# Performance work log

Measured on AMD Instinct MI355X. Metric: run time of the kernel, lower is better.

The kernel has to match this reference:

```python
import jax, jax.numpy as jnp
import numpy as np

D_MODEL = 1024
NUM_HEADS = 16
HEAD_DIM = D_MODEL // NUM_HEADS  # 64
ROPE_THETA = 10000.0
SEQ_LEN = 4096
BATCH = 1


def apply_rope(x, positions, theta=ROPE_THETA):
    # x: [b, h, s, d], positions: [s]
    d = x.shape[-1]
    inv_freq = theta ** (-jnp.arange(0, d, 2, dtype=jnp.float32) / d)  # [d/2]
    angles = positions.astype(jnp.float32)[:, None] * inv_freq[None, :]  # [s, d/2]
    cos = jnp.cos(angles)  # [s, d/2]
    sin = jnp.sin(angles)
    x1 = x[..., 0::2]  # [b, h, s, d/2]
    x2 = x[..., 1::2]
    r1 = x1 * cos - x2 * sin
    r2 = x1 * sin + x2 * cos
    # interleave back to [..., d]
    out = jnp.stack([r1, r2], axis=-1).reshape(x.shape)
    return out.astype(x.dtype)


def setup_inputs() -> dict:
    key = jax.random.key(0)
    k_x, k_qkv, k_o = jax.random.split(key, 3)
    scale_in = 1.0 / np.sqrt(D_MODEL)
    return {
        "x": jax.random.normal(k_x, (BATCH, SEQ_LEN, D_MODEL), dtype=jnp.float32),
        "token_positions": jnp.arange(SEQ_LEN, dtype=jnp.int64 if jax.config.jax_enable_x64 else jnp.int32),
        "w_qkv": jax.random.normal(k_qkv, (3 * D_MODEL, D_MODEL), dtype=jnp.float32) * scale_in,
        "w_o": jax.random.normal(k_o, (D_MODEL, D_MODEL), dtype=jnp.float32) * scale_in,
    }


def reference(x, token_positions, w_qkv, w_o):
    b, s, _ = x.shape
    # QKV projection (Linear without bias, weight [out, in])
    x_qkv = jnp.einsum('bsd,ed->bse', x, w_qkv)  # [b, s, 3*d_model]
    # rearrange 'b s (three heads kv) -> three b heads s kv'
    x_qkv = x_qkv.reshape(b, s, 3, NUM_HEADS, HEAD_DIM)
    x_qkv = jnp.transpose(x_qkv, (2, 0, 3, 1, 4))  # [3, b, h, s, d]
    q, k, v = x_qkv[0], x_qkv[1], x_qkv[2]
    q = apply_rope(q, token_positions)
    k = apply_rope(k, token_positions)
    # scaled dot-product attention with causal mask
    scores = jnp.einsum('bhnd,bhmd->bhnm', q, k) / jnp.sqrt(jnp.float32(HEAD_DIM))
    causal = jnp.tril(jnp.ones((s, s), dtype=bool))  # [s, s]
    scores = jnp.where(causal[None, None], scores, jnp.float32(-jnp.inf))
    weights = jax.nn.softmax(scores, axis=-1)
    attn = jnp.einsum('bhnm,bhmd->bhnd', weights, v)  # [b, h, s, d]
    attn = jnp.transpose(attn, (0, 2, 1, 3)).reshape(b, s, NUM_HEADS * HEAD_DIM)
    return jnp.einsum('bsd,ed->bse', attn, w_o)
```

## Files before the change

kernel.cpp:

```cpp
#include <hip/hip_runtime.h>

#define SEQ 4096
#define DMODEL 1024
#define HEADS 16
#define HD 64
#define NQKV 3072

typedef __attribute__((ext_vector_type(8))) __bf16 bf16x8;
typedef __attribute__((ext_vector_type(4))) __bf16 bf16x4;
typedef __attribute__((ext_vector_type(8))) short short8;
typedef __attribute__((ext_vector_type(4))) float f32x4;
typedef __attribute__((ext_vector_type(16))) float f32x16;
typedef __attribute__((ext_vector_type(4))) unsigned int u32x4;

__device__ __forceinline__ unsigned short f2bf(float f) {
    unsigned u = __builtin_bit_cast(unsigned, f);
    return (unsigned short)((u + 0x7fffu + ((u >> 16) & 1u)) >> 16);
}
__device__ __forceinline__ float bf2f(unsigned short h) {
    return __builtin_bit_cast(float, (unsigned)h << 16);
}
__device__ __forceinline__ unsigned cvt_pk_bf16(float lo, float hi) {
    unsigned r;
    asm("v_cvt_pk_bf16_f32 %0, %1, %2" : "=v"(r) : "v"(lo), "v"(hi));
    return r;
}

__device__ __forceinline__ void gload16(const void* g, void* l) {
    __builtin_amdgcn_global_load_lds(
        (const __attribute__((address_space(1))) unsigned int*)g,
        (__attribute__((address_space(3))) unsigned int*)l, 16, 0, 0);
}

#define TS(qt, kh) (0x40 | ((kh) << 5) | (qt))
__device__ __constant__ unsigned char TASKS[28] = {
    TS(15,0), TS(15,1), TS(14,0), TS(14,1), TS(13,0), TS(13,1),
    TS(12,0), TS(12,1), TS(11,0), TS(11,1), TS(10,0), TS(10,1),
    TS(9,0),  TS(9,1),  TS(8,0),  TS(8,1),  TS(7,0),  TS(7,1),
    3,        TS(6,0),  TS(6,1),  2,        TS(5,0),  TS(5,1),
    TS(4,0),  TS(4,1),  1,        0
};

__global__ void f2bf_all(const float* __restrict__ x, const float* __restrict__ wqkv,
                         const float* __restrict__ wo, unsigned short* __restrict__ dst) {
    const int N0 = SEQ * DMODEL / 4;
    const int N1 = N0 + NQKV * DMODEL / 4;
    const int NT = N1 + DMODEL * DMODEL / 4;
    int i = blockIdx.x * 256 + threadIdx.x;
    int stride = gridDim.x * 256;
    for (; i < NT; i += stride) {
        const float4* src;
        if (i < N0)      src = reinterpret_cast<const float4*>(x) + i;
        else if (i < N1) src = reinterpret_cast<const float4*>(wqkv) + (i - N0);
        else             src = reinterpret_cast<const float4*>(wo) + (i - N1);
        float4 f = *src;
        ushort4 o;
        o.x = f2bf(f.x); o.y = f2bf(f.y); o.z = f2bf(f.z); o.w = f2bf(f.w);
        reinterpret_cast<ushort4*>(dst)[i] = o;
    }
}

template <int EPI>
__global__ __launch_bounds__(256) void gemm_bt(const unsigned short* __restrict__ A,
                                               const unsigned short* __restrict__ B,
                                               float* __restrict__ outF,
                                               unsigned short* __restrict__ outB,
                                               int M, int N, int K) {
    alignas(16) __shared__ unsigned short a_lds[2][128 * 32];
    alignas(16) __shared__ unsigned short b_lds[2][128 * 32];
    const int tid = threadIdx.x;
    const int wave = tid >> 6, lane = tid & 63;
    const int l16 = lane & 15, g = lane >> 4;
    const int wr = wave >> 1, wc = wave & 1;
    const int bm = blockIdx.x, bn = blockIdx.y;

    const int lrow = lane >> 2;
    const int lcol = (lane & 3) * 8;

    const unsigned short* Ag = A + (size_t)(bm * 128 + lrow) * K + lcol;
    const unsigned short* Bg = B + (size_t)(bn * 128 + lrow) * K + lcol;

    f32x4 acc[4][4] = {};
    const int NS = K / 32;

    auto STAGE = [&](int b, int ks) {
#pragma unroll
        for (int j = 0; j < 2; ++j) {
            int chunk = wave * 2 + j;
            gload16(Ag + (size_t)(chunk * 16) * K + ks * 32, a_lds[b] + chunk * 512);
            gload16(Bg + (size_t)(chunk * 16) * K + ks * 32, b_lds[b] + chunk * 512);
        }
    };

    STAGE(0, 0);

    for (int ks = 0; ks < NS; ++ks) {
        const int cur = ks & 1;
        asm volatile("s_waitcnt vmcnt(0)" ::: "memory");
        __builtin_amdgcn_s_barrier();
        if (ks + 1 < NS) STAGE(cur ^ 1, ks + 1);

        bf16x8 af[4], bfr[4];
#pragma unroll
        for (int m = 0; m < 4; ++m)
            af[m] = *reinterpret_cast<const bf16x8*>(a_lds[cur] + (wr * 64 + m * 16 + l16) * 32 + g * 8);
#pragma unroll
        for (int n = 0; n < 4; ++n)
            bfr[n] = *reinterpret_cast<const bf16x8*>(b_lds[cur] + (wc * 64 + n * 16 + l16) * 32 + g * 8);
        __builtin_amdgcn_s_setprio(1);
#pragma unroll
        for (int m = 0; m < 4; ++m)
#pragma unroll
            for (int n = 0; n < 4; ++n)
                acc[m][n] = __builtin_amdgcn_mfma_f32_16x16x32_bf16(af[m], bfr[n], acc[m][n], 0, 0, 0);
        __builtin_amdgcn_s_setprio(0);
    }

#pragma unroll
    for (int m = 0; m < 4; ++m)
#pragma unroll
        for (int n = 0; n < 4; ++n)
#pragma unroll
            for (int r = 0; r < 4; ++r) {
                int row = bm * 128 + wr * 64 + m * 16 + g * 4 + r;
                int col = bn * 128 + wc * 64 + n * 16 + l16;
                float v = acc[m][n][r];
                if (EPI == 0) {
                    int part = col >> 10;
                    int hd = col & 1023;
                    int h = hd >> 6, d = hd & 63;
                    outB[(size_t)((part * HEADS + h) * SEQ + row) * HD + d] = f2bf(v);
                } else {
                    outF[(size_t)row * N + col] = v;
                }
            }
}

__global__ __launch_bounds__(256) void rope_kernel(unsigned short* qkv, const int* __restrict__ pos) {
    int idx = blockIdx.x * 256 + threadIdx.x;
    int chunk = idx & 7;
    int row = idx >> 3;
    int s = row & (SEQ - 1);
    int ph = row >> 12;
    float p = (float)pos[s];
    float scale = (ph < HEADS) ? 0.125f * 1.4426950408889634f : 1.0f;
    unsigned short* base = qkv + ((size_t)ph * SEQ + s) * HD + chunk * 8;
    short8 v = *reinterpret_cast<short8*>(base);
    short8 o;
    const float k = -13.287712379549449f / 32.0f;
#pragma unroll
    for (int j = 0; j < 4; ++j) {
        int i = chunk * 4 + j;
        float ang = p * exp2f((float)i * k);
        float sn, cs;
        sincosf(ang, &sn, &cs);
        float x1 = bf2f((unsigned short)v[2 * j]);
        float x2 = bf2f((unsigned short)v[2 * j + 1]);
        o[2 * j]     = (short)f2bf((x1 * cs - x2 * sn) * scale);
        o[2 * j + 1] = (short)f2bf((x1 * sn + x2 * cs) * scale);
    }
    *reinterpret_cast<short8*>(base) = o;
}

__global__ __launch_bounds__(256) void transpose_v(const unsigned short* __restrict__ qkv,
                                                   unsigned short* __restrict__ vt) {
    const int st = blockIdx.x;
    const int h = blockIdx.y;
    __shared__ unsigned short tile[64][72];
    const unsigned short* Vg = qkv + (size_t)((2 * HEADS + h) * SEQ) * HD;
    const int tid = threadIdx.x;
#pragma unroll
    for (int j = 0; j < 2; ++j) {
        int b = (tid + j * 256) * 8;
        int row = b >> 6;
        int col = b & 63;
        short8 v = *reinterpret_cast<const short8*>(Vg + (size_t)(st * 64 + row) * HD + col);
#pragma unroll
        for (int i = 0; i < 8; ++i) tile[row][col + i] = (unsigned short)v[i];
    }
    __syncthreads();
#pragma unroll
    for (int j = 0; j < 2; ++j) {
        int b = (tid + j * 256) * 8;
        int d = b >> 6;
        int sc = b & 63;
        short8 o;
#pragma unroll
        for (int i = 0; i < 8; ++i) o[i] = (short)tile[sc + i][d];
        *reinterpret_cast<short8*>(vt + (size_t)(h * HD + d) * SEQ + st * 64 + sc) = o;
    }
}

__global__ __launch_bounds__(512) void attn_kernel(const unsigned short* __restrict__ qkv,
                                                   const unsigned short* __restrict__ vt,
                                                   unsigned short* __restrict__ attnout,
                                                   int* __restrict__ qcnt,
                                                   unsigned short* __restrict__ pO,
                                                   float* __restrict__ lmf) {
    const int xcd = blockIdx.x & 7;
    const int tid = threadIdx.x;
    const int wave = tid >> 6, lane = tid & 63;
    const int l32 = lane & 31, hi = lane >> 5;

    alignas(16) __shared__ unsigned short k_lds[2][128 * 64];
    alignas(16) __shared__ unsigned short v_lds[2][2][64 * 64];
    __shared__ int slot_sh;

    const int rsw = (l32 & 7) << 4;

    for (;;) {
        if (tid == 0) slot_sh = atomicAdd(&qcnt[xcd], 1);
        __syncthreads();
        const int t = slot_sh;
        __syncthreads();
        if (t >= 56) break;

        const int hloc = t & 1;
        const unsigned char e = TASKS[t >> 1];
        const int qtile = e & 31;
        const int khalf = (e >> 5) & 1;
        const bool isSplit = (e >> 6) != 0;
        const int T = 2 * qtile + 2, Hh = qtile + 1;
        const int k0 = isSplit ? (khalf ? Hh : 0) : 0;
        const int k1 = isSplit ? (khalf ? T : Hh) : T;
        const int h = xcd * 2 + hloc;

        const unsigned short* Qg = qkv + (size_t)((0 * HEADS + h) * SEQ) * HD;
        const unsigned short* Kg = qkv + (size_t)((1 * HEADS + h) * SEQ) * HD;
        const unsigned short* VTg = vt + (size_t)h * HD * SEQ;

        const int qbase = qtile * 256 + wave * 32;
        const int qrow = qbase + l32;

        bf16x8 qf[4];
#pragma unroll
        for (int dg = 0; dg < 4; ++dg)
            qf[dg] = *reinterpret_cast<const bf16x8*>(Qg + (size_t)qrow * HD + dg * 16 + hi * 8);

        f32x16 oa[2] = {};
        float m_r = -1e30f, l_r = 0.f;

        auto STAGE = [&](int b, int kt) {
#pragma unroll
            for (int i = 0; i < 2; ++i) {
                int base = wave * 2048 + i * 1024;
                int byte = base + lane * 16;
                int krow = byte >> 7;
                int kc8 = ((byte >> 4) & 7) ^ (krow & 7);
                gload16(Kg + (size_t)(kt * 128 + krow) * HD + kc8 * 8, (char*)k_lds[b] + base);
                int fr = byte >> 7;
                int h64 = fr >> 6, vd = fr & 63;
                int vc8 = ((byte >> 4) & 7) ^ (vd & 7);
                gload16(VTg + (size_t)vd * SEQ + kt * 128 + h64 * 64 + vc8 * 8,
                        (char*)v_lds[b] + base);
            }
        };

        STAGE(0, k0);

        for (int kt = k0; kt < k1; ++kt) {
            const int cur = (kt - k0) & 1;
            asm volatile("s_waitcnt vmcnt(0)" ::: "memory");
            __builtin_amdgcn_s_barrier();
            if (kt + 1 < k1) STAGE(cur ^ 1, kt + 1);

#pragma unroll
            for (int hh = 0; hh < 2; ++hh) {
                if (hh && (kt * 128 + 64) > (qbase + 31)) break;

                f32x16 s[2] = {};
                __builtin_amdgcn_s_setprio(1);
#pragma unroll
                for (int g = 0; g < 2; ++g) {
                    int row = hh * 64 + g * 32 + l32;
#pragma unroll
                    for (int dg = 0; dg < 4; ++dg) {
                        bf16x8 kf = *reinterpret_cast<const bf16x8*>(
                            (char*)k_lds[cur] + row * 128 + ((dg * 32 + hi * 16) ^ rsw));
                        s[g] = __builtin_amdgcn_mfma_f32_32x32x16_bf16(kf, qf[dg], s[g], 0, 0, 0);
                    }
                }
                __builtin_amdgcn_s_setprio(0);

                if (kt * 128 + hh * 64 + 63 > qbase) {
#pragma unroll
                    for (int g = 0; g < 2; ++g)
#pragma unroll
                        for (int r = 0; r < 16; ++r) {
                            int kv = kt * 128 + hh * 64 + g * 32 + (r & 3) + 8 * (r >> 2) + 4 * hi;
                            if (kv > qrow) s[g][r] = -1e30f;
                        }
                }

                float ma = -1e30f, mb = -1e30f, mc = -1e30f, md = -1e30f;
#pragma unroll
                for (int r = 0; r < 16; r += 4) {
                    ma = fmaxf(ma, fmaxf(s[0][r], s[1][r]));
                    mb = fmaxf(mb, fmaxf(s[0][r + 1], s[1][r + 1]));
                    mc = fmaxf(mc, fmaxf(s[0][r + 2], s[1][r + 2]));
                    md = fmaxf(md, fmaxf(s[0][r + 3], s[1][r + 3]));
                }
                float mx = fmaxf(fmaxf(ma, mb), fmaxf(mc, md));
                mx = fmaxf(mx, __shfl_xor(mx, 32));

                if (__any(mx > m_r + 8.0f)) {
                    float mnew = fmaxf(m_r, mx);
                    float alpha = __builtin_amdgcn_exp2f(m_r - mnew);
                    m_r = mnew;
#pragma unroll
                    for (int r = 0; r < 16; ++r) { oa[0][r] *= alpha; oa[1][r] *= alpha; }
                    l_r *= alpha;
                }

#pragma unroll
                for (int g = 0; g < 2; ++g)
#pragma unroll
                    for (int r = 0; r < 16; ++r) s[g][r] = __builtin_amdgcn_exp2f(s[g][r] - m_r);

                float ra = 0.f, rb = 0.f;
#pragma unroll
                for (int r = 0; r < 16; r += 2) {
                    ra += s[0][r] + s[1][r];
                    rb += s[0][r + 1] + s[1][r + 1];
                }
                float rs = ra + rb;
                rs += __shfl_xor(rs, 32);
                l_r += rs;

                __builtin_amdgcn_s_setprio(1);
#pragma unroll
                for (int g = 0; g < 2; ++g) {
                    u32x4 pfw[2];
#pragma unroll
                    for (int u = 0; u < 2; ++u) {
                        unsigned wA = cvt_pk_bf16(s[g][8 * u + 0], s[g][8 * u + 1]);
                        unsigned wC = cvt_pk_bf16(s[g][8 * u + 2], s[g][8 * u + 3]);
                        unsigned wB = cvt_pk_bf16(s[g][8 * u + 4], s[g][8 * u + 5]);
                        unsigned wD = cvt_pk_bf16(s[g][8 * u + 6], s[g][8 * u + 7]);
                        unsigned wAx = __shfl_xor((int)wA, 32), wBx = __shfl_xor((int)wB, 32);
                        unsigned wCx = __shfl_xor((int)wC, 32), wDx = __shfl_xor((int)wD, 32);
                        pfw[u][0] = hi ? wBx : wA;
                        pfw[u][1] = hi ? wDx : wC;
                        pfw[u][2] = hi ? wB : wAx;
                        pfw[u][3] = hi ? wD : wCx;
                    }
#pragma unroll
                    for (int u = 0; u < 2; ++u) {
                        bf16x8 pf = __builtin_bit_cast(bf16x8, pfw[u]);
                        int ks = g * 2 + u;
#pragma unroll
                        for (int dg = 0; dg < 2; ++dg) {
                            bf16x8 vf = *reinterpret_cast<const bf16x8*>(
                                (char*)v_lds[cur][hh] + (dg * 32 + l32) * 128 + ((ks * 32 + hi * 16) ^ rsw));
                            oa[dg] = __builtin_amdgcn_mfma_f32_32x32x16_bf16(vf, pf, oa[dg], 0, 0, 0);
                        }
                    }
                }
                __builtin_amdgcn_s_setprio(0);
            }
        }

        const int ql = wave * 32 + l32;
        if (isSplit) {
            int sidx = (h * 12 + (qtile - 4)) * 2 + khalf;
            unsigned short* Op = pO + (size_t)sidx * 16384;
#pragma unroll
            for (int dg = 0; dg < 2; ++dg)
#pragma unroll
                for (int rq = 0; rq < 4; ++rq) {
                    ushort4 ov;
                    ov.x = f2bf(oa[dg][4 * rq + 0]);
                    ov.y = f2bf(oa[dg][4 * rq + 1]);
                    ov.z = f2bf(oa[dg][4 * rq + 2]);
                    ov.w = f2bf(oa[dg][4 * rq + 3]);
                    *reinterpret_cast<ushort4*>(Op + ql * 64 + dg * 32 + 8 * rq + 4 * hi) = ov;
                }
            if (hi == 0) {
                lmf[sidx * 512 + ql] = l_r;
                lmf[sidx * 512 + 256 + ql] = m_r;
            }
        } else {
            float inv = 1.0f / l_r;
            unsigned short* orow = attnout + (size_t)(qtile * 256 + ql) * DMODEL + h * HD;
#pragma unroll
            for (int dg = 0; dg < 2; ++dg)
#pragma unroll
                for (int rq = 0; rq < 4; ++rq) {
                    ushort4 ov;
                    ov.x = f2bf(oa[dg][4 * rq + 0] * inv);
                    ov.y = f2bf(oa[dg][4 * rq + 1] * inv);
                    ov.z = f2bf(oa[dg][4 * rq + 2] * inv);
                    ov.w = f2bf(oa[dg][4 * rq + 3] * inv);
                    *reinterpret_cast<ushort4*>(orow + dg * 32 + 8 * rq + 4 * hi) = ov;
                }
        }
    }
}

__global__ __launch_bounds__(256) void merge_kernel(const unsigned short* __restrict__ pO,
                                                    const float* __restrict__ lmf,
                                                    unsigned short* __restrict__ attnout) {
    int idx = blockIdx.x * 256 + threadIdx.x;
    if (idx >= 16 * 12 * 2048) return;
    int h = idx / (12 * 2048);
    int r = idx % (12 * 2048);
    int qt = r >> 11;
    int rr = r & 2047;
    int q = rr >> 3, d8 = rr & 7;

    int s0 = (h * 12 + qt) * 2;
    float l0 = lmf[s0 * 512 + q],       m0 = lmf[s0 * 512 + 256 + q];
    float l1 = lmf[(s0 + 1) * 512 + q], m1 = lmf[(s0 + 1) * 512 + 256 + q];
    float m = fmaxf(m0, m1);
    float a0 = __builtin_amdgcn_exp2f(m0 - m), a1 = __builtin_amdgcn_exp2f(m1 - m);
    float L = l0 * a0 + l1 * a1;
    float c0 = a0 / L, c1 = a1 / L;

    const unsigned short* O0 = pO + (size_t)s0 * 16384 + q * 64 + d8 * 8;
    const unsigned short* O1 = O0 + 16384;
    short8 v0 = *reinterpret_cast<const short8*>(O0);
    short8 v1 = *reinterpret_cast<const short8*>(O1);
    short8 o;
#pragma unroll
    for (int j = 0; j < 8; ++j) {
        float val = bf2f((unsigned short)v0[j]) * c0 + bf2f((unsigned short)v1[j]) * c1;
        o[j] = (short)f2bf(val);
    }
    int qtile = qt + 4;
    *reinterpret_cast<short8*>(attnout + (size_t)(qtile * 256 + q) * DMODEL + h * HD + d8 * 8) = o;
}

extern "C" void kernel_launch(void* const* d_in, const int* in_sizes, int n_in,
                              void* d_out, int out_size, void* d_ws, size_t ws_size,
                              hipStream_t stream) {
    const float* x = (const float*)d_in[0];
    const int* pos = (const int*)d_in[1];
    const float* wqkv = (const float*)d_in[2];
    const float* wo = (const float*)d_in[3];
    float* out = (float*)d_out;

    unsigned short* xb = (unsigned short*)d_ws;
    unsigned short* wqkvb = xb + (size_t)SEQ * DMODEL;
    unsigned short* wob = wqkvb + (size_t)NQKV * DMODEL;
    unsigned short* qkvp = wob + (size_t)DMODEL * DMODEL;
    unsigned short* vt = qkvp + (size_t)3 * HEADS * SEQ * HD;
    unsigned short* attnb = vt + (size_t)HEADS * HD * SEQ;

    char* sbase = (char*)d_ws;
    int* qcnt = (int*)sbase;
    float* lmf = (float*)(sbase + 1024);
    unsigned short* pO = (unsigned short*)(sbase + (1 << 20));

    f2bf_all<<<2048, 256, 0, stream>>>(x, wqkv, wo, xb);

    dim3 g1(SEQ / 128, NQKV / 128);
    gemm_bt<0><<<g1, 256, 0, stream>>>(xb, wqkvb, nullptr, qkvp, SEQ, NQKV, DMODEL);

    rope_kernel<<<(2 * HEADS * SEQ * 8) / 256, 256, 0, stream>>>(qkvp, pos);
    transpose_v<<<dim3(SEQ / 64, HEADS), 256, 0, stream>>>(qkvp, vt);

    hipMemsetAsync(qcnt, 0, 64, stream);
    attn_kernel<<<512, 512, 0, stream>>>(qkvp, vt, attnb, qcnt, pO, lmf);
    merge_kernel<<<(16 * 12 * 2048 + 255) / 256, 256, 0, stream>>>(pO, lmf, attnb);

    dim3 g2(SEQ / 128, DMODEL / 128);
    gemm_bt<1><<<g2, 256, 0, stream>>>(attnb, wob, out, nullptr, SEQ, DMODEL, DMODEL);
}
```

Before: 147.2 us.

## Fuse RoPE and V transpose into QKV GEMM epilogue with precomputed sin/cos

Removes the separate rope and transpose_v kernels by applying RoPE (with the Q scale) directly to fp32 accumulators in the QKV GEMM epilogue, pairing adjacent columns with a lane shuffle. V tiles are transposed through a small LDS buffer and written straight into the transposed layout. Sin/cos tables are precomputed in the conversion kernel. This saves two launches and a full read/write of the Q, K and V buffers, and RoPE now rounds once from fp32 instead of twice. In exchange the epilogue does more per-element table loads and scattered 2-byte stores, and the V path has no barrier around the per-wave LDS tile.

```diff
diff --git a/kernel.cpp b/kernel.cpp
--- a/kernel.cpp
+++ b/kernel.cpp
@@ -42,7 +42,9 @@
 };
 
 __global__ void f2bf_all(const float* __restrict__ x, const float* __restrict__ wqkv,
-                         const float* __restrict__ wo, unsigned short* __restrict__ dst) {
+                         const float* __restrict__ wo, const int* __restrict__ pos,
+                         unsigned short* __restrict__ dst,
+                         float* __restrict__ csT, float* __restrict__ snT) {
     const int N0 = SEQ * DMODEL / 4;
     const int N1 = N0 + NQKV * DMODEL / 4;
     const int NT = N1 + DMODEL * DMODEL / 4;
@@ -58,6 +60,16 @@
         o.x = f2bf(f.x); o.y = f2bf(f.y); o.z = f2bf(f.z); o.w = f2bf(f.w);
         reinterpret_cast<ushort4*>(dst)[i] = o;
     }
+    const float kk = -13.287712379549449f / 32.0f;
+    for (int idx = blockIdx.x * 256 + threadIdx.x; idx < SEQ * 32; idx += stride) {
+        int s = idx >> 5, fi = idx & 31;
+        float p = (float)pos[s];
+        float ang = p * exp2f((float)fi * kk);
+        float sn_, cs_;
+        sincosf(ang, &sn_, &cs_);
+        csT[idx] = cs_;
+        snT[idx] = sn_;
+    }
 }
 
 template <int EPI>
@@ -65,9 +77,13 @@
                                                const unsigned short* __restrict__ B,
                                                float* __restrict__ outF,
                                                unsigned short* __restrict__ outB,
+                                               unsigned short* __restrict__ vtp,
+                                               const float* __restrict__ csT,
+                                               const float* __restrict__ snT,
                                                int M, int N, int K) {
     alignas(16) __shared__ unsigned short a_lds[2][128 * 32];
     alignas(16) __shared__ unsigned short b_lds[2][128 * 32];
+    __shared__ unsigned short vtile[4][16][72];
     const int tid = threadIdx.x;
     const int wave = tid >> 6, lane = tid & 63;
     const int l16 = lane & 15, g = lane >> 4;
@@ -116,78 +132,55 @@
         __builtin_amdgcn_s_setprio(0);
     }
 
-#pragma unroll
-    for (int m = 0; m < 4; ++m)
-#pragma unroll
-        for (int n = 0; n < 4; ++n)
-#pragma unroll
-            for (int r = 0; r < 4; ++r) {
-                int row = bm * 128 + wr * 64 + m * 16 + g * 4 + r;
-                int col = bn * 128 + wc * 64 + n * 16 + l16;
-                float v = acc[m][n][r];
-                if (EPI == 0) {
-                    int part = col >> 10;
-                    int hd = col & 1023;
-                    int h = hd >> 6, d = hd & 63;
-                    outB[(size_t)((part * HEADS + h) * SEQ + row) * HD + d] = f2bf(v);
-                } else {
-                    outF[(size_t)row * N + col] = v;
+    if (EPI == 0) {
+        const float QS = 0.125f * 1.4426950408889634f;
+#pragma unroll
+        for (int n = 0; n < 4; ++n) {
+            const int col = bn * 128 + wc * 64 + n * 16 + l16;
+            const int part = col >> 10;
+            const int hh = (col >> 6) & 15;
+            const int d = n * 16 + l16;
+            if (part < 2) {
+                const int fi = (col & 63) >> 1;
+                const float sc = (part == 0) ? QS : 1.0f;
+                const bool odd = (col & 1) != 0;
+#pragma unroll
+                for (int m = 0; m < 4; ++m)
+#pragma unroll
+                    for (int r = 0; r < 4; ++r) {
+                        int row = bm * 128 + wr * 64 + m * 16 + g * 4 + r;
+                        float v = acc[m][n][r];
+                        float pp = __shfl_xor(v, 1);
+                        float cs_ = csT[row * 32 + fi];
+                        float sn_ = snT[row * 32 + fi];
+                        float out = odd ? (pp * sn_ + v * cs_) : (v * cs_ - pp * sn_);
+                        outB[(size_t)((part * HEADS + hh) * SEQ + row) * HD + (col & 63)] = f2bf(out * sc);
+                    }
+            } else {
+#pragma unroll
+                for (int m = 0; m < 4; ++m)
+#pragma unroll
+                    for (int r = 0; r < 4; ++r)
+                        vtile[wave][l16][m * 16 + g * 4 + r] = f2bf(acc[m][n][r]);
+#pragma unroll
+                for (int dd = 0; dd < 16; ++dd) {
+                    int dg = ((col & 63) & ~15) + dd;
+                    vtp[(size_t)(hh * HD + dg) * SEQ + bm * 128 + wr * 64 + lane] =
+                        vtile[wave][dd][lane];
                 }
             }
-}
-
-__global__ __launch_bounds__(256) void rope_kernel(unsigned short* qkv, const int* __restrict__ pos) {
-    int idx = blockIdx.x * 256 + threadIdx.x;
-    int chunk = idx & 7;
-    int row = idx >> 3;
-    int s = row & (SEQ - 1);
-    int ph = row >> 12;
-    float p = (float)pos[s];
-    float scale = (ph < HEADS) ? 0.125f * 1.4426950408889634f : 1.0f;
-    unsigned short* base = qkv + ((size_t)ph * SEQ + s) * HD + chunk * 8;
-    short8 v = *reinterpret_cast<short8*>(base);
-    short8 o;
-    const float k = -13.287712379549449f / 32.0f;
-#pragma unroll
-    for (int j = 0; j < 4; ++j) {
-        int i = chunk * 4 + j;
-        float ang = p * exp2f((float)i * k);
-        float sn, cs;
-        sincosf(ang, &sn, &cs);
-        float x1 = bf2f((unsigned short)v[2 * j]);
-        float x2 = bf2f((unsigned short)v[2 * j + 1]);
-        o[2 * j]     = (short)f2bf((x1 * cs - x2 * sn) * scale);
-        o[2 * j + 1] = (short)f2bf((x1 * sn + x2 * cs) * scale);
-    }
-    *reinterpret_cast<short8*>(base) = o;
-}
-
-__global__ __launch_bounds__(256) void transpose_v(const unsigned short* __restrict__ qkv,
-                                                   unsigned short* __restrict__ vt) {
-    const int st = blockIdx.x;
-    const int h = blockIdx.y;
-    __shared__ unsigned short tile[64][72];
-    const unsigned short* Vg = qkv + (size_t)((2 * HEADS + h) * SEQ) * HD;
-    const int tid = threadIdx.x;
-#pragma unroll
-    for (int j = 0; j < 2; ++j) {
-        int b = (tid + j * 256) * 8;
-        int row = b >> 6;
-        int col = b & 63;
-        short8 v = *reinterpret_cast<const short8*>(Vg + (size_t)(st * 64 + row) * HD + col);
-#pragma unroll
-        for (int i = 0; i < 8; ++i) tile[row][col + i] = (unsigned short)v[i];
-    }
-    __syncthreads();
-#pragma unroll
-    for (int j = 0; j < 2; ++j) {
-        int b = (tid + j * 256) * 8;
-        int d = b >> 6;
-        int sc = b & 63;
-        short8 o;
-#pragma unroll
-        for (int i = 0; i < 8; ++i) o[i] = (short)tile[sc + i][d];
-        *reinterpret_cast<short8*>(vt + (size_t)(h * HD + d) * SEQ + st * 64 + sc) = o;
+        }
+    } else {
+#pragma unroll
+        for (int m = 0; m < 4; ++m)
+#pragma unroll
+            for (int n = 0; n < 4; ++n)
+#pragma unroll
+                for (int r = 0; r < 4; ++r) {
+                    int row = bm * 128 + wr * 64 + m * 16 + g * 4 + r;
+                    int col = bn * 128 + wc * 64 + n * 16 + l16;
+                    outF[(size_t)row * N + col] = acc[m][n][r];
+                }
     }
 }
 
@@ -443,26 +436,25 @@
     unsigned short* wqkvb = xb + (size_t)SEQ * DMODEL;
     unsigned short* wob = wqkvb + (size_t)NQKV * DMODEL;
     unsigned short* qkvp = wob + (size_t)DMODEL * DMODEL;
-    unsigned short* vt = qkvp + (size_t)3 * HEADS * SEQ * HD;
-    unsigned short* attnb = vt + (size_t)HEADS * HD * SEQ;
+    unsigned short* vtp = qkvp + (size_t)2 * HEADS * SEQ * HD;
+    float* csT = (float*)(qkvp + (size_t)3 * HEADS * SEQ * HD);
+    float* snT = csT + SEQ * 32;
+    unsigned short* attnb = (unsigned short*)(snT + SEQ * 32);
 
     char* sbase = (char*)d_ws;
     int* qcnt = (int*)sbase;
     float* lmf = (float*)(sbase + 1024);
     unsigned short* pO = (unsigned short*)(sbase + (1 << 20));
 
-    f2bf_all<<<2048, 256, 0, stream>>>(x, wqkv, wo, xb);
+    f2bf_all<<<2048, 256, 0, stream>>>(x, wqkv, wo, pos, xb, csT, snT);
 
     dim3 g1(SEQ / 128, NQKV / 128);
-    gemm_bt<0><<<g1, 256, 0, stream>>>(xb, wqkvb, nullptr, qkvp, SEQ, NQKV, DMODEL);
-
-    rope_kernel<<<(2 * HEADS * SEQ * 8) / 256, 256, 0, stream>>>(qkvp, pos);
-    transpose_v<<<dim3(SEQ / 64, HEADS), 256, 0, stream>>>(qkvp, vt);
+    gemm_bt<0><<<g1, 256, 0, stream>>>(xb, wqkvb, nullptr, qkvp, vtp, csT, snT, SEQ, NQKV, DMODEL);
 
     hipMemsetAsync(qcnt, 0, 64, stream);
-    attn_kernel<<<512, 512, 0, stream>>>(qkvp, vt, attnb, qcnt, pO, lmf);
+    attn_kernel<<<512, 512, 0, stream>>>(qkvp, vtp, attnb, qcnt, pO, lmf);
     merge_kernel<<<(16 * 12 * 2048 + 255) / 256, 256, 0, stream>>>(pO, lmf, attnb);
 
     dim3 g2(SEQ / 128, DMODEL / 128);
-    gemm_bt<1><<<g2, 256, 0, stream>>>(attnb, wob, out, nullptr, SEQ, DMODEL, DMODEL);
-}
+    gemm_bt<1><<<g2, 256, 0, stream>>>(attnb, wob, out, nullptr, nullptr, nullptr, nullptr, SEQ, DMODEL, DMODEL);
+}
```

Measured after the change: 137.6 us. 1.07x faster.
